# Kernel tuning notes

Hardware: AMD Instinct MI355X
Metric: run time of the kernel (lower is better)

## Reference

```python
import jax, jax.numpy as jnp
import numpy as np

NP, NQ = 8192, 8192
DP, DQ = 512, 512
D1, D2 = 256, 256
DEG = 32  # avg degree for synthetic bipartite adjacency


def setup_inputs() -> dict:
    key = jax.random.key(0)
    ks = list(jax.random.split(key, 40))
    it = iter(ks)

    def nk():
        return next(it)

    hp = jax.random.normal(nk(), (NP, DP), jnp.float32)
    hq = jax.random.normal(nk(), (NQ, DQ), jnp.float32)

    def adj(shape):
        # sparse-ish binary adjacency, ~DEG neighbors per row
        return (jax.random.uniform(nk(), shape) < DEG / shape[1]).astype(jnp.float32)

    a_cons = adj((NP, NQ))
    a_prod = adj((NQ, NP))
    a_rev_cons = adj((NQ, NP))
    a_rev_prod = adj((NP, NQ))

    def lin(din, dout):
        s = (6.0 / (din + dout)) ** 0.5  # xavier_uniform, gain=1
        w = jax.random.uniform(nk(), (dout, din), jnp.float32, minval=-s, maxval=s)
        return w, jnp.zeros((dout,), jnp.float32)

    d = dict(hp=hp, hq=hq, a_cons=a_cons, a_prod=a_prod,
             a_rev_cons=a_rev_cons, a_rev_prod=a_rev_prod)
    d['wp1_w'], d['wp1_b'] = lin(DP, D1)
    d['wq1_w'], d['wq1_b'] = lin(DQ, D1)
    d['wcons1_w'], d['wcons1_b'] = lin(DQ, D1)
    d['wrprod1_w'], d['wrprod1_b'] = lin(DQ, D1)
    d['wprod1_w'], d['wprod1_b'] = lin(DP, D1)
    d['wrcons1_w'], d['wrcons1_b'] = lin(DP, D1)
    d['wp2_w'], d['wp2_b'] = lin(D1, D2)
    d['wq2_w'], d['wq2_b'] = lin(D1, D2)
    d['wcons2_w'], d['wcons2_b'] = lin(D1, D2)
    d['wrprod2_w'], d['wrprod2_b'] = lin(D1, D2)
    d['wprod2_w'], d['wprod2_b'] = lin(D1, D2)
    d['wrcons2_w'], d['wrcons2_b'] = lin(D1, D2)
    return d


def reference(hp, hq, a_cons, a_prod, a_rev_cons, a_rev_prod,
              wp1_w, wp1_b, wq1_w, wq1_b, wcons1_w, wcons1_b,
              wrprod1_w, wrprod1_b, wprod1_w, wprod1_b, wrcons1_w, wrcons1_b,
              wp2_w, wp2_b, wq2_w, wq2_b, wcons2_w, wcons2_b,
              wrprod2_w, wrprod2_b, wprod2_w, wprod2_b, wrcons2_w, wrcons2_b):
    lin = lambda x, w, b: x @ w.T + b
    act = lambda x: jax.nn.leaky_relu(x, 0.1)
    # layer 1 (dropout is identity in eval mode)
    hp1 = act(lin(hp, wp1_w, wp1_b)
              + a_cons @ lin(hq, wcons1_w, wcons1_b)
              + a_rev_prod @ lin(hq, wrprod1_w, wrprod1_b))
    hq1 = act(lin(hq, wq1_w, wq1_b)
              + a_prod @ lin(hp, wprod1_w, wprod1_b)
              + a_rev_cons @ lin(hp, wrcons1_w, wrcons1_b))
    # layer 2
    hp2 = act(lin(hp1, wp2_w, wp2_b)
              + a_cons @ lin(hq1, wcons2_w, wcons2_b)
              + a_rev_prod @ lin(hq1, wrprod2_w, wrprod2_b))
    hq2 = act(lin(hq1, wq2_w, wq2_b)
              + a_prod @ lin(hp1, wprod2_w, wprod2_b)
              + a_rev_cons @ lin(hp1, wrcons2_w, wrcons2_b))
    norm = lambda x: x / (jnp.linalg.norm(x, axis=1, keepdims=True) + 1e-9)
    return norm(hp2), norm(hq2)
```

## Files before the change

kernel.cpp:

```cpp
#include <hip/hip_runtime.h>

#define CAP 128

typedef __attribute__((ext_vector_type(8))) short bf16x8;
typedef __attribute__((ext_vector_type(4))) float f32x4;
typedef __attribute__((ext_vector_type(4))) float f32x4v;

__device__ __forceinline__ unsigned short f2bf(float f) {
    unsigned u = __float_as_uint(f);
    u += 0x7FFFu + ((u >> 16) & 1u);
    return (unsigned short)(u >> 16);
}
__device__ __forceinline__ float bf2f(unsigned short h) {
    return __uint_as_float(((unsigned)h) << 16);
}

struct CvtSeg { const float* s; unsigned short* d; int n4; };
struct CvtArgs { CvtSeg seg[14]; };

__global__ __launch_bounds__(256) void cvt_kernel(CvtArgs c) {
    int gid = blockIdx.x * 256 + threadIdx.x;
    int stride = gridDim.x * 256;
    #pragma unroll
    for (int si = 0; si < 14; ++si) {
        CvtSeg sg = c.seg[si];
        for (int i = gid; i < sg.n4; i += stride) {
            float4 v = ((const float4*)sg.s)[i];
            ushort4 o;
            o.x = f2bf(v.x); o.y = f2bf(v.y); o.z = f2bf(v.z); o.w = f2bf(v.w);
            ((ushort4*)sg.d)[i] = o;
        }
    }
}

struct ExtArgs { const float* a0; const float* a1; const float* a2; const float* a3; int* idx; int* cnt; };

__global__ __launch_bounds__(256) void extract_kernel(ExtArgs e) {
    int row = blockIdx.x, m = blockIdx.y, t = threadIdx.x;
    int wave = t >> 6, lane = t & 63;
    const float* A = (m == 0) ? e.a0 : (m == 1) ? e.a1 : (m == 2) ? e.a2 : e.a3;
    const f32x4v* rp = (const f32x4v*)(A + (size_t)row * 8192);
    unsigned mask = 0;
    #pragma unroll
    for (int it = 0; it < 8; ++it) {
        f32x4v v = __builtin_nontemporal_load(&rp[it * 256 + t]);
        mask |= (unsigned)(v.x != 0.f) << (4 * it);
        mask |= (unsigned)(v.y != 0.f) << (4 * it + 1);
        mask |= (unsigned)(v.z != 0.f) << (4 * it + 2);
        mask |= (unsigned)(v.w != 0.f) << (4 * it + 3);
    }
    int cnt = __popc(mask);
    int pre = cnt;
    #pragma unroll
    for (int off = 1; off < 64; off <<= 1) {
        int u = __shfl_up(pre, off);
        if (lane >= off) pre += u;
    }
    __shared__ int lwt[4];
    if (lane == 63) lwt[wave] = pre;
    __syncthreads();
    int wbase = 0;
    if (wave > 0) wbase += lwt[0];
    if (wave > 1) wbase += lwt[1];
    if (wave > 2) wbase += lwt[2];
    int o = wbase + pre - cnt;
    int* op = e.idx + ((size_t)m * 8192 + row) * CAP;
    while (mask) {
        int b = __ffs((int)mask) - 1;
        mask &= mask - 1;
        int j = (b >> 2) * 1024 + t * 4 + (b & 3);
        if (o < CAP) op[o] = j;
        o++;
    }
    if (t == 0) {
        int tot = lwt[0] + lwt[1] + lwt[2] + lwt[3];
        e.cnt[m * 8192 + row] = tot < CAP ? tot : CAP;
    }
}

struct GemmDesc { const unsigned short* X; const unsigned short* W; const float* bias; unsigned short* Z; };
struct GemmArgs { GemmDesc d[6]; };

template<int K>
__global__ __launch_bounds__(256) void gemm6_kernel(GemmArgs ga) {
    GemmDesc g = ga.d[blockIdx.z];
    int wave = threadIdx.x >> 6;
    int lane = threadIdx.x & 63;
    int r = lane & 15, q = lane >> 4;
    int rowbase = blockIdx.x * 128 + wave * 32;
    int colbase = blockIdx.y * 64;
    f32x4 acc[2][4] = {};
    const unsigned short* xp0 = g.X + (size_t)(rowbase + r) * K + q * 8;
    const unsigned short* xp1 = xp0 + (size_t)16 * K;
    const unsigned short* wbase = g.W + (size_t)(colbase + r) * K + q * 8;
    #pragma unroll
    for (int k0 = 0; k0 < K; k0 += 32) {
        bf16x8 a0 = *(const bf16x8*)(xp0 + k0);
        bf16x8 a1 = *(const bf16x8*)(xp1 + k0);
        #pragma unroll
        for (int nt = 0; nt < 4; ++nt) {
            bf16x8 b = *(const bf16x8*)(wbase + (size_t)nt * 16 * K + k0);
            acc[0][nt] = __builtin_amdgcn_mfma_f32_16x16x32_bf16(a0, b, acc[0][nt], 0, 0, 0);
            acc[1][nt] = __builtin_amdgcn_mfma_f32_16x16x32_bf16(a1, b, acc[1][nt], 0, 0, 0);
        }
    }
    #pragma unroll
    for (int mt = 0; mt < 2; ++mt) {
        #pragma unroll
        for (int nt = 0; nt < 4; ++nt) {
            int col = colbase + nt * 16 + r;
            float bv = g.bias[col];
            #pragma unroll
            for (int j = 0; j < 4; ++j) {
                int row = rowbase + mt * 16 + q * 4 + j;
                g.Z[(size_t)row * 256 + col] = f2bf(acc[mt][nt][j] + bv);
            }
        }
    }
}

struct AggSide {
    const unsigned short* zself;
    const unsigned short* za;
    const unsigned short* zb;
    const int* idxa; const int* cnta;
    const int* idxb; const int* cntb;
    unsigned short* out_bf;
    float* out_f;
};

template<int FINAL>
__global__ __launch_bounds__(256) void agg_kernel(AggSide s0, AggSide s1) {
    AggSide s = blockIdx.y ? s1 : s0;
    int t = threadIdx.x;
    int l32 = t & 31;
    int row = blockIdx.x * 8 + (t >> 5);
    int c8 = l32 * 8;
    bf16x8 v = *(const bf16x8*)(s.zself + (size_t)row * 256 + c8);
    float acc[8];
    #pragma unroll
    for (int j = 0; j < 8; ++j) acc[j] = bf2f((unsigned short)v[j]);
    int ca = s.cnta[row], cb = s.cntb[row];
    const int* ia = s.idxa + (size_t)row * CAP;
    const int* ib = s.idxb + (size_t)row * CAP;
    #pragma unroll 4
    for (int k = 0; k < ca; ++k) {
        int na = ia[k];
        bf16x8 w = *(const bf16x8*)(s.za + (size_t)na * 256 + c8);
        #pragma unroll
        for (int j = 0; j < 8; ++j) acc[j] += bf2f((unsigned short)w[j]);
    }
    #pragma unroll 4
    for (int k = 0; k < cb; ++k) {
        int nb = ib[k];
        bf16x8 w = *(const bf16x8*)(s.zb + (size_t)nb * 256 + c8);
        #pragma unroll
        for (int j = 0; j < 8; ++j) acc[j] += bf2f((unsigned short)w[j]);
    }
    #pragma unroll
    for (int j = 0; j < 8; ++j) acc[j] = acc[j] > 0.f ? acc[j] : 0.1f * acc[j];
    if (FINAL) {
        float ss = 0.f;
        #pragma unroll
        for (int j = 0; j < 8; ++j) ss += acc[j] * acc[j];
        #pragma unroll
        for (int off = 1; off < 32; off <<= 1) ss += __shfl_xor(ss, off);
        float sc = 1.0f / (sqrtf(ss) + 1e-9f);
        float4 o0, o1;
        o0.x = acc[0] * sc; o0.y = acc[1] * sc; o0.z = acc[2] * sc; o0.w = acc[3] * sc;
        o1.x = acc[4] * sc; o1.y = acc[5] * sc; o1.z = acc[6] * sc; o1.w = acc[7] * sc;
        float* op = s.out_f + (size_t)row * 256 + c8;
        *(float4*)op = o0;
        *(float4*)(op + 4) = o1;
    } else {
        bf16x8 o;
        #pragma unroll
        for (int j = 0; j < 8; ++j) o[j] = (short)f2bf(acc[j]);
        *(bf16x8*)(s.out_bf + (size_t)row * 256 + c8) = o;
    }
}

extern "C" void kernel_launch(void* const* d_in, const int* in_sizes, int n_in,
                              void* d_out, int out_size, void* d_ws, size_t ws_size,
                              hipStream_t stream) {
    const float* hp         = (const float*)d_in[0];
    const float* hq         = (const float*)d_in[1];
    const float* a_cons     = (const float*)d_in[2];
    const float* a_prod     = (const float*)d_in[3];
    const float* a_rev_cons = (const float*)d_in[4];
    const float* a_rev_prod = (const float*)d_in[5];

    char* ws = (char*)d_ws;
    constexpr size_t SZ_H   = (size_t)8192 * 512 * 2;
    constexpr size_t SZ_W1  = (size_t)256 * 512 * 2;
    constexpr size_t SZ_W2  = (size_t)256 * 256 * 2;
    constexpr size_t SZ_Z   = (size_t)8192 * 256 * 2;
    constexpr size_t OFF_HP  = 0;
    constexpr size_t OFF_HQ  = OFF_HP + SZ_H;
    constexpr size_t OFF_WBF = OFF_HQ + SZ_H;
    constexpr size_t OFF_IDX = OFF_WBF + 6 * SZ_W1 + 6 * SZ_W2;
    constexpr size_t OFF_CNT = OFF_IDX + (size_t)4 * 8192 * CAP * 4;
    constexpr size_t OFF_Z   = OFF_CNT + (size_t)4 * 8192 * 4;
    constexpr size_t OFF_H1P = OFF_Z + 6 * SZ_Z;
    constexpr size_t OFF_H1Q = OFF_H1P + SZ_Z;

    unsigned short* hp_bf = (unsigned short*)(ws + OFF_HP);
    unsigned short* hq_bf = (unsigned short*)(ws + OFF_HQ);
    int* idx = (int*)(ws + OFF_IDX);
    int* cnt = (int*)(ws + OFF_CNT);
    unsigned short* z[6];
    for (int i = 0; i < 6; ++i) z[i] = (unsigned short*)(ws + OFF_Z + i * SZ_Z);
    unsigned short* h1p = (unsigned short*)(ws + OFF_H1P);
    unsigned short* h1q = (unsigned short*)(ws + OFF_H1Q);

    unsigned short* wbf[12];
    for (int i = 0; i < 6; ++i) wbf[i]     = (unsigned short*)(ws + OFF_WBF + i * SZ_W1);
    for (int i = 0; i < 6; ++i) wbf[6 + i] = (unsigned short*)(ws + OFF_WBF + 6 * SZ_W1 + i * SZ_W2);

    CvtArgs ca;
    ca.seg[0] = { hp, hp_bf, 8192 * 512 / 4 };
    ca.seg[1] = { hq, hq_bf, 8192 * 512 / 4 };
    const int wIdxL1[6] = { 6, 10, 12, 8, 14, 16 };
    const int wIdxL2[6] = { 18, 22, 24, 20, 26, 28 };
    for (int i = 0; i < 6; ++i) ca.seg[2 + i] = { (const float*)d_in[wIdxL1[i]], wbf[i],     256 * 512 / 4 };
    for (int i = 0; i < 6; ++i) ca.seg[8 + i] = { (const float*)d_in[wIdxL2[i]], wbf[6 + i], 256 * 256 / 4 };
    cvt_kernel<<<dim3(1024), dim3(256), 0, stream>>>(ca);

    ExtArgs ea = { a_cons, a_prod, a_rev_cons, a_rev_prod, idx, cnt };
    extract_kernel<<<dim3(8192, 4), dim3(256), 0, stream>>>(ea);

    GemmArgs g1;
    g1.d[0] = { hp_bf, wbf[0], (const float*)d_in[7],  z[0] };
    g1.d[1] = { hq_bf, wbf[1], (const float*)d_in[11], z[1] };
    g1.d[2] = { hq_bf, wbf[2], (const float*)d_in[13], z[2] };
    g1.d[3] = { hq_bf, wbf[3], (const float*)d_in[9],  z[3] };
    g1.d[4] = { hp_bf, wbf[4], (const float*)d_in[15], z[4] };
    g1.d[5] = { hp_bf, wbf[5], (const float*)d_in[17], z[5] };
    gemm6_kernel<512><<<dim3(64, 4, 6), dim3(256), 0, stream>>>(g1);

    int* idx0 = idx + (size_t)0 * 8192 * CAP;
    int* idx1 = idx + (size_t)1 * 8192 * CAP;
    int* idx2 = idx + (size_t)2 * 8192 * CAP;
    int* idx3 = idx + (size_t)3 * 8192 * CAP;
    int* cnt0 = cnt, *cnt1 = cnt + 8192, *cnt2 = cnt + 16384, *cnt3 = cnt + 24576;

    AggSide p1 = { z[0], z[1], z[2], idx0, cnt0, idx3, cnt3, h1p, nullptr };
    AggSide q1 = { z[3], z[4], z[5], idx1, cnt1, idx2, cnt2, h1q, nullptr };
    agg_kernel<0><<<dim3(1024, 2), dim3(256), 0, stream>>>(p1, q1);

    GemmArgs g2;
    g2.d[0] = { h1p, wbf[6],  (const float*)d_in[19], z[0] };
    g2.d[1] = { h1q, wbf[7],  (const float*)d_in[23], z[1] };
    g2.d[2] = { h1q, wbf[8],  (const float*)d_in[25], z[2] };
    g2.d[3] = { h1q, wbf[9],  (const float*)d_in[21], z[3] };
    g2.d[4] = { h1p, wbf[10], (const float*)d_in[27], z[4] };
    g2.d[5] = { h1p, wbf[11], (const float*)d_in[29], z[5] };
    gemm6_kernel<256><<<dim3(64, 4, 6), dim3(256), 0, stream>>>(g2);

    float* outp = (float*)d_out;
    AggSide p2 = { z[0], z[1], z[2], idx0, cnt0, idx3, cnt3, nullptr, outp };
    AggSide q2 = { z[3], z[4], z[5], idx1, cnt1, idx2, cnt2, nullptr, outp + (size_t)8192 * 256 };
    agg_kernel<1><<<dim3(1024, 2), dim3(256), 0, stream>>>(p2, q2);
}
```

Baseline: 373.5 us.

## Fuse adjacency extraction with layer-1 GEMM in one interleaved launch

Merges the bandwidth-bound adjacency-to-index extraction kernel and the compute-bound layer-1 six-way GEMM into a single kernel. Blocks are interleaved so one GEMM block follows every eight extract blocks, letting MFMA work overlap with streaming the dense adjacency reads. The GEMM tile shrinks to 128x32 to produce more, smaller blocks, which lowers per-block data reuse. The launch bound now requests high occupancy.

After: 370.3 us. No clear change (-0.9%).

```diff
diff --git a/kernel.cpp b/kernel.cpp
--- a/kernel.cpp
+++ b/kernel.cpp
@@ -35,8 +35,8 @@
 
 struct ExtArgs { const float* a0; const float* a1; const float* a2; const float* a3; int* idx; int* cnt; };
 
-__global__ __launch_bounds__(256) void extract_kernel(ExtArgs e) {
-    int row = blockIdx.x, m = blockIdx.y, t = threadIdx.x;
+__device__ __forceinline__ void extract_body(const ExtArgs& e, int row, int m) {
+    int t = threadIdx.x;
     int wave = t >> 6, lane = t & 63;
     const float* A = (m == 0) ? e.a0 : (m == 1) ? e.a1 : (m == 2) ? e.a2 : e.a3;
     const f32x4v* rp = (const f32x4v*)(A + (size_t)row * 8192);
@@ -82,6 +82,62 @@
 struct GemmArgs { GemmDesc d[6]; };
 
 template<int K>
+__device__ __forceinline__ void gemm_slim_body(const GemmArgs& ga, int bx, int by, int bz) {
+    GemmDesc g = ga.d[bz];
+    int wave = threadIdx.x >> 6;
+    int lane = threadIdx.x & 63;
+    int r = lane & 15, q = lane >> 4;
+    int rowbase = bx * 128 + wave * 32;
+    int colbase = by * 32;
+    f32x4 acc[2][2] = {};
+    const unsigned short* xp0 = g.X + (size_t)(rowbase + r) * K + q * 8;
+    const unsigned short* xp1 = xp0 + (size_t)16 * K;
+    const unsigned short* wb0 = g.W + (size_t)(colbase + r) * K + q * 8;
+    const unsigned short* wb1 = wb0 + (size_t)16 * K;
+    #pragma unroll 4
+    for (int k0 = 0; k0 < K; k0 += 32) {
+        bf16x8 a0 = *(const bf16x8*)(xp0 + k0);
+        bf16x8 a1 = *(const bf16x8*)(xp1 + k0);
+        bf16x8 b0 = *(const bf16x8*)(wb0 + k0);
+        bf16x8 b1 = *(const bf16x8*)(wb1 + k0);
+        acc[0][0] = __builtin_amdgcn_mfma_f32_16x16x32_bf16(a0, b0, acc[0][0], 0, 0, 0);
+        acc[0][1] = __builtin_amdgcn_mfma_f32_16x16x32_bf16(a0, b1, acc[0][1], 0, 0, 0);
+        acc[1][0] = __builtin_amdgcn_mfma_f32_16x16x32_bf16(a1, b0, acc[1][0], 0, 0, 0);
+        acc[1][1] = __builtin_amdgcn_mfma_f32_16x16x32_bf16(a1, b1, acc[1][1], 0, 0, 0);
+    }
+    #pragma unroll
+    for (int mt = 0; mt < 2; ++mt) {
+        #pragma unroll
+        for (int nt = 0; nt < 2; ++nt) {
+            int col = colbase + nt * 16 + r;
+            float bv = g.bias[col];
+            #pragma unroll
+            for (int j = 0; j < 4; ++j) {
+                int row = rowbase + mt * 16 + q * 4 + j;
+                g.Z[(size_t)row * 256 + col] = f2bf(acc[mt][nt][j] + bv);
+            }
+        }
+    }
+}
+
+__global__ __launch_bounds__(256, 8) void fused_ext_gemm_kernel(ExtArgs e, GemmArgs ga) {
+    int bid = blockIdx.x;
+    int gemmIdx = -1, extIdx;
+    if (bid < 27648) {
+        int grp = bid / 9, rem = bid % 9;
+        if (rem == 0) gemmIdx = grp;
+        extIdx = grp * 8 + (rem - 1);
+    } else {
+        extIdx = 24576 + (bid - 27648);
+    }
+    if (gemmIdx >= 0) {
+        gemm_slim_body<512>(ga, gemmIdx & 63, (gemmIdx >> 6) & 7, gemmIdx >> 9);
+    } else {
+        extract_body(e, extIdx & 8191, extIdx >> 13);
+    }
+}
+
+template<int K>
 __global__ __launch_bounds__(256) void gemm6_kernel(GemmArgs ga) {
     GemmDesc g = ga.d[blockIdx.z];
     int wave = threadIdx.x >> 6;
@@ -227,8 +283,6 @@
     cvt_kernel<<<dim3(1024), dim3(256), 0, stream>>>(ca);
 
     ExtArgs ea = { a_cons, a_prod, a_rev_cons, a_rev_prod, idx, cnt };
-    extract_kernel<<<dim3(8192, 4), dim3(256), 0, stream>>>(ea);
-
     GemmArgs g1;
     g1.d[0] = { hp_bf, wbf[0], (const float*)d_in[7],  z[0] };
     g1.d[1] = { hq_bf, wbf[1], (const float*)d_in[11], z[1] };
@@ -236,7 +290,7 @@
     g1.d[3] = { hq_bf, wbf[3], (const float*)d_in[9],  z[3] };
     g1.d[4] = { hp_bf, wbf[4], (const float*)d_in[15], z[4] };
     g1.d[5] = { hp_bf, wbf[5], (const float*)d_in[17], z[5] };
-    gemm6_kernel<512><<<dim3(64, 4, 6), dim3(256), 0, stream>>>(g1);
+    fused_ext_gemm_kernel<<<dim3(35840), dim3(256), 0, stream>>>(ea, g1);
 
     int* idx0 = idx + (size_t)0 * 8192 * CAP;
     int* idx1 = idx + (size_t)1 * 8192 * CAP;
```

## Stage GEMM tiles through swizzled LDS with 128x128 block tiles

Applied to the files above, without the earlier changes.

Replaces the register-only GEMM, which loads A and B fragments straight from global memory, with a kernel that cooperatively stages 128x64 tiles of X and W into LDS using an XOR swizzle. Each wave then computes a 64x64 sub-tile with MFMA. The aim is to cut redundant global loads of the weight and activation tiles by sharing them across waves. In exchange it adds two barriers per K step, has no double buffering, and halves the grid along the column axis.

After: 308.6 us. 17.4% less time.

```diff
diff --git a/kernel.cpp b/kernel.cpp
--- a/kernel.cpp
+++ b/kernel.cpp
@@ -82,39 +82,63 @@
 struct GemmArgs { GemmDesc d[6]; };
 
 template<int K>
-__global__ __launch_bounds__(256) void gemm6_kernel(GemmArgs ga) {
+__global__ __launch_bounds__(256) void gemm_lds_kernel(GemmArgs ga) {
     GemmDesc g = ga.d[blockIdx.z];
-    int wave = threadIdx.x >> 6;
-    int lane = threadIdx.x & 63;
+    __shared__ unsigned short Asm[128 * 64];
+    __shared__ unsigned short Bsm[128 * 64];
+    int t = threadIdx.x;
+    int wave = t >> 6, lane = t & 63;
     int r = lane & 15, q = lane >> 4;
-    int rowbase = blockIdx.x * 128 + wave * 32;
-    int colbase = blockIdx.y * 64;
-    f32x4 acc[2][4] = {};
-    const unsigned short* xp0 = g.X + (size_t)(rowbase + r) * K + q * 8;
-    const unsigned short* xp1 = xp0 + (size_t)16 * K;
-    const unsigned short* wbase = g.W + (size_t)(colbase + r) * K + q * 8;
-    #pragma unroll
-    for (int k0 = 0; k0 < K; k0 += 32) {
-        bf16x8 a0 = *(const bf16x8*)(xp0 + k0);
-        bf16x8 a1 = *(const bf16x8*)(xp1 + k0);
-        #pragma unroll
-        for (int nt = 0; nt < 4; ++nt) {
-            bf16x8 b = *(const bf16x8*)(wbase + (size_t)nt * 16 * K + k0);
-            acc[0][nt] = __builtin_amdgcn_mfma_f32_16x16x32_bf16(a0, b, acc[0][nt], 0, 0, 0);
-            acc[1][nt] = __builtin_amdgcn_mfma_f32_16x16x32_bf16(a1, b, acc[1][nt], 0, 0, 0);
-        }
-    }
-    #pragma unroll
-    for (int mt = 0; mt < 2; ++mt) {
-        #pragma unroll
-        for (int nt = 0; nt < 4; ++nt) {
-            int col = colbase + nt * 16 + r;
-            float bv = g.bias[col];
-            #pragma unroll
-            for (int j = 0; j < 4; ++j) {
-                int row = rowbase + mt * 16 + q * 4 + j;
-                g.Z[(size_t)row * 256 + col] = f2bf(acc[mt][nt][j] + bv);
+    int wr = wave >> 1, wc = wave & 1;
+    int rowbase = blockIdx.x * 128;
+    int colbase = blockIdx.y * 128;
+    const unsigned short* gA[4];
+    const unsigned short* gB[4];
+    int ls[4];
+    #pragma unroll
+    for (int i = 0; i < 4; ++i) {
+        int s = t + 256 * i;
+        int srow = s >> 3, c = s & 7;
+        gA[i] = g.X + (size_t)(rowbase + srow) * K + c * 8;
+        gB[i] = g.W + (size_t)(colbase + srow) * K + c * 8;
+        ls[i] = srow * 64 + ((c ^ (srow & 7)) * 8);
+    }
+    f32x4 acc[4][4] = {};
+    for (int k0 = 0; k0 < K; k0 += 64) {
+        #pragma unroll
+        for (int i = 0; i < 4; ++i) {
+            *(bf16x8*)&Asm[ls[i]] = *(const bf16x8*)(gA[i] + k0);
+            *(bf16x8*)&Bsm[ls[i]] = *(const bf16x8*)(gB[i] + k0);
+        }
+        __syncthreads();
+        #pragma unroll
+        for (int ks = 0; ks < 2; ++ks) {
+            bf16x8 af[4], bfr[4];
+            #pragma unroll
+            for (int m = 0; m < 4; ++m)
+                af[m] = *(const bf16x8*)&Asm[(wr * 64 + m * 16 + r) * 64 + (((ks * 4 + q) ^ (r & 7)) * 8)];
+            #pragma unroll
+            for (int n = 0; n < 4; ++n)
+                bfr[n] = *(const bf16x8*)&Bsm[(wc * 64 + n * 16 + r) * 64 + (((ks * 4 + q) ^ (r & 7)) * 8)];
+            #pragma unroll
+            for (int m = 0; m < 4; ++m) {
+                #pragma unroll
+                for (int n = 0; n < 4; ++n)
+                    acc[m][n] = __builtin_amdgcn_mfma_f32_16x16x32_bf16(af[m], bfr[n], acc[m][n], 0, 0, 0);
             }
+        }
+        __syncthreads();
+    }
+    #pragma unroll
+    for (int n = 0; n < 4; ++n) {
+        int col = colbase + wc * 64 + n * 16 + r;
+        float bv = g.bias[col];
+        #pragma unroll
+        for (int m = 0; m < 4; ++m) {
+            int rowb = rowbase + wr * 64 + m * 16 + q * 4;
+            #pragma unroll
+            for (int j = 0; j < 4; ++j)
+                g.Z[(size_t)(rowb + j) * 256 + col] = f2bf(acc[m][n][j] + bv);
         }
     }
 }
@@ -236,7 +260,7 @@
     g1.d[3] = { hq_bf, wbf[3], (const float*)d_in[9],  z[3] };
     g1.d[4] = { hp_bf, wbf[4], (const float*)d_in[15], z[4] };
     g1.d[5] = { hp_bf, wbf[5], (const float*)d_in[17], z[5] };
-    gemm6_kernel<512><<<dim3(64, 4, 6), dim3(256), 0, stream>>>(g1);
+    gemm_lds_kernel<512><<<dim3(64, 2, 6), dim3(256), 0, stream>>>(g1);
 
     int* idx0 = idx + (size_t)0 * 8192 * CAP;
     int* idx1 = idx + (size_t)1 * 8192 * CAP;
@@ -255,7 +279,7 @@
     g2.d[3] = { h1q, wbf[9],  (const float*)d_in[21], z[3] };
     g2.d[4] = { h1p, wbf[10], (const float*)d_in[27], z[4] };
     g2.d[5] = { h1p, wbf[11], (const float*)d_in[29], z[5] };
-    gemm6_kernel<256><<<dim3(64, 4, 6), dim3(256), 0, stream>>>(g2);
+    gemm_lds_kernel<256><<<dim3(64, 2, 6), dim3(256), 0, stream>>>(g2);
 
     float* outp = (float*)d_out;
     AggSide p2 = { z[0], z[1], z[2], idx0, cnt0, idx3, cnt3, nullptr, outp };
```
